# Performance work log

Measured on AMD Instinct MI355X. Metric: run time of the kernel, lower is better.

Reference implementation:

```python
import jax, jax.numpy as jnp
import numpy as np

B, S, D = 32, 4096, 64          # batch, max seq len, input_dim
P, STRIDE, H = 8, 4, 512        # patch_size, patch_stride, hidden_size
T = (S - P) // STRIDE + 1       # static max token count (sample 0 has length S)
EPS = 1e-6


def setup_inputs() -> dict:
    key = jax.random.key(0)
    k1, k2, k3 = jax.random.split(key, 3)
    x = jax.random.normal(k1, (B, S, D), dtype=jnp.float32)
    lengths = jax.random.randint(k2, (B,), P, S + 1)
    lengths = lengths.at[0].set(S)  # at least one full-length sample -> max_tokens == T
    W = jax.random.normal(k3, (P * D, H), dtype=jnp.float32) / np.sqrt(P * D)
    b = jnp.zeros((H,), dtype=jnp.float32)
    scale = jnp.ones((H,), dtype=jnp.float32)  # RMSNorm scale
    return {"x": x, "lengths": lengths, "W": W, "b": b, "scale": scale}


def _patch(x, lengths):
    # number of tokens per sample: len(range(0, max(L-P+1, 1), STRIDE))
    n_tok = jnp.where(lengths >= P, (lengths - P) // STRIDE + 1, 1)  # [B]
    # gather positions for every (token, within-patch) slot
    pos = jnp.arange(T)[:, None] * STRIDE + jnp.arange(P)[None, :]   # [T, P]
    tokens = x[:, pos, :]                                            # [B, T, P, D]
    valid = (pos[None, :, :] < lengths[:, None, None]) \
          & (jnp.arange(T)[None, :, None] < n_tok[:, None, None])    # [B, T, P]
    tokens = jnp.where(valid[..., None], tokens, 0.0)
    return tokens.reshape(B, T, P * D), n_tok


def reference(x, lengths, W, b, scale):
    tokens, token_lengths = _patch(x, lengths)        # [B, T, P*D], [B]
    h = tokens @ W + b                                # proj -> [B, T, H]
    rms = jnp.sqrt(jnp.mean(h * h, axis=-1, keepdims=True) + EPS)
    hidden = h / rms * scale                          # RMSNorm
    return hidden, token_lengths, tokens
```

## Files before the change

### kernel.cpp

```cpp
#include <hip/hip_runtime.h>
#include <hip/hip_bf16.h>

constexpr int Bc = 32, Sc = 4096, Dc = 64, Pc = 8, STRIDEc = 4, Hc = 512;
constexpr int Tc = (Sc - Pc) / STRIDEc + 1;
constexpr int Kc = Pc * Dc;
constexpr float EPSc = 1e-6f;
constexpr int PITCH = 40;

typedef __bf16 bf16x8 __attribute__((ext_vector_type(8)));
typedef unsigned short ushort8 __attribute__((ext_vector_type(8)));
typedef float f32x4 __attribute__((ext_vector_type(4)));

__device__ __forceinline__ int n_tok_of(int len) {
    return (len >= Pc) ? ((len - Pc) / STRIDEc + 1) : 1;
}

__device__ __forceinline__ unsigned short f2bf(float f) {
    unsigned u = __builtin_bit_cast(unsigned, f);
    u = (u + 0x7FFFu + ((u >> 16) & 1u)) >> 16;
    return (unsigned short)u;
}

__global__ __launch_bounds__(256) void prep_kernel(
        const float* __restrict__ W, const int* __restrict__ lengths,
        unsigned short* __restrict__ Wt, float* __restrict__ out_tl) {
    __shared__ float tile[32][33];
    const int k0 = blockIdx.x * 32, n0 = blockIdx.y * 32;
    const int r = threadIdx.x >> 3, c = (threadIdx.x & 7) * 4;
    const float4 v = *(const float4*)(W + (size_t)(k0 + r) * Hc + n0 + c);
    tile[c + 0][r] = v.x;
    tile[c + 1][r] = v.y;
    tile[c + 2][r] = v.z;
    tile[c + 3][r] = v.w;
    __syncthreads();
    ushort4 o;
    o.x = f2bf(tile[r][c + 0]);
    o.y = f2bf(tile[r][c + 1]);
    o.z = f2bf(tile[r][c + 2]);
    o.w = f2bf(tile[r][c + 3]);
    *(ushort4*)(Wt + (size_t)blockIdx.x * (Hc * 32) + (size_t)(n0 + r) * 32 + c) = o;
    if (blockIdx.x == 0 && blockIdx.y == 0 && threadIdx.x < Bc)
        out_tl[threadIdx.x] = (float)n_tok_of(lengths[threadIdx.x]);
}

__global__ __launch_bounds__(256, 2) void fused_kernel(
        const float* __restrict__ x, const int* __restrict__ lengths,
        const unsigned short* __restrict__ Wt, const float* __restrict__ bias,
        const float* __restrict__ scale, float* __restrict__ hidden,
        float* __restrict__ tokens) {
    const int b  = blockIdx.y;
    const int t0 = blockIdx.x * 64;
    const int len = lengths[b];
    const int ntok = n_tok_of(len);

    __shared__ unsigned short As[64 * PITCH];
    __shared__ unsigned short Bs[512 * PITCH];
    __shared__ float ssbuf[4][64];

    const int tid  = threadIdx.x;
    const int w    = tid >> 6;
    const int lane = tid & 63;
    const int l15  = lane & 15;
    const int quad = lane >> 4;

    f32x4 acc[4][8];
#pragma unroll
    for (int tt = 0; tt < 4; ++tt)
#pragma unroll
        for (int ct = 0; ct < 8; ++ct) acc[tt][ct] = (f32x4){0.f, 0.f, 0.f, 0.f};

    const float* xb   = x + (size_t)b * (Sc * Dc);
    float*       tokb = tokens + (size_t)b * Tc * Kc;

    int   a_r[2], a_c[2];  bool a_tv[2];  const float* a_src[2];
#pragma unroll
    for (int it = 0; it < 2; ++it) {
        const int l = tid + it * 256;
        a_r[it] = l >> 3;
        a_c[it] = (l & 7) * 4;
        const int t = t0 + a_r[it];
        a_tv[it] = (t < Tc);
        a_src[it] = xb + (size_t)t * (STRIDEc * Dc);
    }

    float4  ra[2];
    ushort8 rb[8];

#pragma unroll
    for (int it = 0; it < 2; ++it) {
        const int t = t0 + a_r[it];
        const int kk = a_c[it];
        const int pos = t * STRIDEc + (kk >> 6);
        ra[it] = make_float4(0.f, 0.f, 0.f, 0.f);
        if (a_tv[it] && t < ntok && pos < len) ra[it] = *(const float4*)(a_src[it] + kk);
    }
#pragma unroll
    for (int it = 0; it < 8; ++it)
        rb[it] = *(const ushort8*)(Wt + (size_t)(tid + it * 256) * 8);

    for (int step = 0; step < 16; ++step) {
        const int k0 = step * 32;
        if (step) __syncthreads();

#pragma unroll
        for (int it = 0; it < 2; ++it) {
            const float4 v = ra[it];
            if (a_tv[it])
                *(float4*)(tokb + (size_t)(t0 + a_r[it]) * Kc + k0 + a_c[it]) = v;
            ushort4 h4;
            h4.x = f2bf(v.x); h4.y = f2bf(v.y); h4.z = f2bf(v.z); h4.w = f2bf(v.w);
            *(ushort4*)(As + a_r[it] * PITCH + a_c[it]) = h4;
        }
#pragma unroll
        for (int it = 0; it < 8; ++it) {
            const int cc = tid + it * 256;
            *(ushort8*)(Bs + (cc >> 2) * PITCH + (cc & 3) * 8) = rb[it];
        }
        __syncthreads();

        if (step < 15) {
            const int kn = k0 + 32;
#pragma unroll
            for (int it = 0; it < 2; ++it) {
                const int t = t0 + a_r[it];
                const int kk = kn + a_c[it];
                const int pos = t * STRIDEc + (kk >> 6);
                ra[it] = make_float4(0.f, 0.f, 0.f, 0.f);
                if (a_tv[it] && t < ntok && pos < len)
                    ra[it] = *(const float4*)(a_src[it] + kk);
            }
            const unsigned short* wsrc = Wt + (size_t)(step + 1) * (Hc * 32);
#pragma unroll
            for (int it = 0; it < 8; ++it)
                rb[it] = *(const ushort8*)(wsrc + (size_t)(tid + it * 256) * 8);
        }

        bf16x8 btok[4];
#pragma unroll
        for (int tt = 0; tt < 4; ++tt)
            btok[tt] = __builtin_bit_cast(bf16x8,
                *(const ushort8*)(As + (tt * 16 + l15) * PITCH + quad * 8));
#pragma unroll
        for (int ct = 0; ct < 8; ++ct) {
            bf16x8 aW = __builtin_bit_cast(bf16x8,
                *(const ushort8*)(Bs + (w * 128 + ct * 16 + l15) * PITCH + quad * 8));
#pragma unroll
            for (int tt = 0; tt < 4; ++tt)
                acc[tt][ct] = __builtin_amdgcn_mfma_f32_16x16x32_bf16(
                    aW, btok[tt], acc[tt][ct], 0, 0, 0);
        }
    }

    float ss[4] = {0.f, 0.f, 0.f, 0.f};
#pragma unroll
    for (int ct = 0; ct < 8; ++ct) {
        const f32x4 b4 = *(const f32x4*)(bias + w * 128 + ct * 16 + quad * 4);
#pragma unroll
        for (int tt = 0; tt < 4; ++tt) {
            f32x4 h = acc[tt][ct] + b4;
            acc[tt][ct] = h;
            ss[tt] += h[0] * h[0] + h[1] * h[1] + h[2] * h[2] + h[3] * h[3];
        }
    }
#pragma unroll
    for (int tt = 0; tt < 4; ++tt) {
        float s = ss[tt];
        s += __shfl_xor(s, 16);
        s += __shfl_xor(s, 32);
        if (quad == 0) ssbuf[w][tt * 16 + l15] = s;
    }
    __syncthreads();
    float rstd[4];
#pragma unroll
    for (int tt = 0; tt < 4; ++tt) {
        const int r = tt * 16 + l15;
        const float tot = ssbuf[0][r] + ssbuf[1][r] + ssbuf[2][r] + ssbuf[3][r];
        rstd[tt] = rsqrtf(tot * (1.0f / (float)Hc) + EPSc);
    }
#pragma unroll
    for (int ct = 0; ct < 8; ++ct) {
        const f32x4 s4 = *(const f32x4*)(scale + w * 128 + ct * 16 + quad * 4);
#pragma unroll
        for (int tt = 0; tt < 4; ++tt) {
            const int t = t0 + tt * 16 + l15;
            if (t < Tc) {
                f32x4 o = acc[tt][ct] * rstd[tt] * s4;
                *(f32x4*)(hidden + ((size_t)b * Tc + t) * Hc
                          + w * 128 + ct * 16 + quad * 4) = o;
            }
        }
    }
}

extern "C" void kernel_launch(void* const* d_in, const int* in_sizes, int n_in,
                              void* d_out, int out_size, void* d_ws, size_t ws_size,
                              hipStream_t stream) {
    const float* x       = (const float*)d_in[0];
    const int*   lengths = (const int*)d_in[1];
    const float* W       = (const float*)d_in[2];
    const float* bias    = (const float*)d_in[3];
    const float* scale   = (const float*)d_in[4];

    const size_t BTH = (size_t)Bc * Tc * Hc;
    float* out    = (float*)d_out;
    float* hidden = out;
    float* tl     = out + BTH;
    float* tokens = out + BTH + Bc;

    unsigned short* Wt = (unsigned short*)d_ws;

    {
        dim3 grid(Hc / 32, Hc / 32);
        prep_kernel<<<grid, 256, 0, stream>>>(W, lengths, Wt, tl);
    }
    {
        dim3 grid(16, Bc);
        fused_kernel<<<grid, 256, 0, stream>>>(x, lengths, Wt, bias, scale,
                                               hidden, tokens);
    }
}
```

Measured before the change: 181.9 us.

## Load MFMA fragments directly from global memory, dropping LDS staging and barriers

```diff
diff --git a/kernel.cpp b/kernel.cpp
--- a/kernel.cpp
+++ b/kernel.cpp
@@ -5,11 +5,11 @@
 constexpr int Tc = (Sc - Pc) / STRIDEc + 1;
 constexpr int Kc = Pc * Dc;
 constexpr float EPSc = 1e-6f;
-constexpr int PITCH = 40;
 
 typedef __bf16 bf16x8 __attribute__((ext_vector_type(8)));
 typedef unsigned short ushort8 __attribute__((ext_vector_type(8)));
 typedef float f32x4 __attribute__((ext_vector_type(4)));
+typedef unsigned int uint4v __attribute__((ext_vector_type(4)));
 
 __device__ __forceinline__ int n_tok_of(int len) {
     return (len >= Pc) ? ((len - Pc) / STRIDEc + 1) : 1;
@@ -20,10 +20,13 @@
     u = (u + 0x7FFFu + ((u >> 16) & 1u)) >> 16;
     return (unsigned short)u;
 }
+__device__ __forceinline__ unsigned pk2bf(float lo, float hi) {
+    return (unsigned)f2bf(lo) | ((unsigned)f2bf(hi) << 16);
+}
 
 __global__ __launch_bounds__(256) void prep_kernel(
         const float* __restrict__ W, const int* __restrict__ lengths,
-        unsigned short* __restrict__ Wt, float* __restrict__ out_tl) {
+        unsigned short* __restrict__ Wfrag, float* __restrict__ out_tl) {
     __shared__ float tile[32][33];
     const int k0 = blockIdx.x * 32, n0 = blockIdx.y * 32;
     const int r = threadIdx.x >> 3, c = (threadIdx.x & 7) * 4;
@@ -38,14 +41,23 @@
     o.y = f2bf(tile[r][c + 1]);
     o.z = f2bf(tile[r][c + 2]);
     o.w = f2bf(tile[r][c + 3]);
-    *(ushort4*)(Wt + (size_t)blockIdx.x * (Hc * 32) + (size_t)(n0 + r) * 32 + c) = o;
+    const int n   = n0 + r;
+    const int kk  = k0 + c;
+    const int wv  = n >> 7;
+    const int ct  = (n >> 4) & 7;
+    const int l15 = n & 15;
+    const int stp = kk >> 5;
+    const int qd  = (kk >> 3) & 3;
+    const size_t off =
+        ((((size_t)stp * 4 + wv) * 8 + ct) * 64 + qd * 16 + l15) * 8 + (kk & 7);
+    *(ushort4*)(Wfrag + off) = o;
     if (blockIdx.x == 0 && blockIdx.y == 0 && threadIdx.x < Bc)
         out_tl[threadIdx.x] = (float)n_tok_of(lengths[threadIdx.x]);
 }
 
 __global__ __launch_bounds__(256, 2) void fused_kernel(
         const float* __restrict__ x, const int* __restrict__ lengths,
-        const unsigned short* __restrict__ Wt, const float* __restrict__ bias,
+        const unsigned short* __restrict__ Wfrag, const float* __restrict__ bias,
         const float* __restrict__ scale, float* __restrict__ hidden,
         float* __restrict__ tokens) {
     const int b  = blockIdx.y;
@@ -53,8 +65,6 @@
     const int len = lengths[b];
     const int ntok = n_tok_of(len);
 
-    __shared__ unsigned short As[64 * PITCH];
-    __shared__ unsigned short Bs[512 * PITCH];
     __shared__ float ssbuf[4][64];
 
     const int tid  = threadIdx.x;
@@ -72,82 +82,68 @@
     const float* xb   = x + (size_t)b * (Sc * Dc);
     float*       tokb = tokens + (size_t)b * Tc * Kc;
 
-    int   a_r[2], a_c[2];  bool a_tv[2];  const float* a_src[2];
+    int a_r[2], a_c[2];
 #pragma unroll
     for (int it = 0; it < 2; ++it) {
         const int l = tid + it * 256;
         a_r[it] = l >> 3;
         a_c[it] = (l & 7) * 4;
-        const int t = t0 + a_r[it];
-        a_tv[it] = (t < Tc);
-        a_src[it] = xb + (size_t)t * (STRIDEc * Dc);
-    }
-
-    float4  ra[2];
-    ushort8 rb[8];
-
-#pragma unroll
-    for (int it = 0; it < 2; ++it) {
-        const int t = t0 + a_r[it];
-        const int kk = a_c[it];
-        const int pos = t * STRIDEc + (kk >> 6);
-        ra[it] = make_float4(0.f, 0.f, 0.f, 0.f);
-        if (a_tv[it] && t < ntok && pos < len) ra[it] = *(const float4*)(a_src[it] + kk);
-    }
-#pragma unroll
-    for (int it = 0; it < 8; ++it)
-        rb[it] = *(const ushort8*)(Wt + (size_t)(tid + it * 256) * 8);
+    }
+    int ft[4];
+#pragma unroll
+    for (int tt = 0; tt < 4; ++tt) ft[tt] = t0 + tt * 16 + l15;
+
+    const unsigned short* wf = Wfrag + ((size_t)w * 8) * 512 + (size_t)lane * 8;
 
     for (int step = 0; step < 16; ++step) {
         const int k0 = step * 32;
-        if (step) __syncthreads();
 
 #pragma unroll
         for (int it = 0; it < 2; ++it) {
-            const float4 v = ra[it];
-            if (a_tv[it])
-                *(float4*)(tokb + (size_t)(t0 + a_r[it]) * Kc + k0 + a_c[it]) = v;
-            ushort4 h4;
-            h4.x = f2bf(v.x); h4.y = f2bf(v.y); h4.z = f2bf(v.z); h4.w = f2bf(v.w);
-            *(ushort4*)(As + a_r[it] * PITCH + a_c[it]) = h4;
-        }
-#pragma unroll
-        for (int it = 0; it < 8; ++it) {
-            const int cc = tid + it * 256;
-            *(ushort8*)(Bs + (cc >> 2) * PITCH + (cc & 3) * 8) = rb[it];
-        }
-        __syncthreads();
-
-        if (step < 15) {
-            const int kn = k0 + 32;
-#pragma unroll
-            for (int it = 0; it < 2; ++it) {
-                const int t = t0 + a_r[it];
-                const int kk = kn + a_c[it];
-                const int pos = t * STRIDEc + (kk >> 6);
-                ra[it] = make_float4(0.f, 0.f, 0.f, 0.f);
-                if (a_tv[it] && t < ntok && pos < len)
-                    ra[it] = *(const float4*)(a_src[it] + kk);
+            const int t = t0 + a_r[it];
+            const int kk = k0 + a_c[it];
+            const int pos = t * STRIDEc + (kk >> 6);
+            float4 v = make_float4(0.f, 0.f, 0.f, 0.f);
+            if (t < ntok && pos < len)
+                v = *(const float4*)(xb + (size_t)t * (STRIDEc * Dc) + kk);
+            if (t < Tc)
+                *(float4*)(tokb + (size_t)t * Kc + kk) = v;
+        }
+
+        ushort8 aW[8];
+        const unsigned short* wfs = wf + (size_t)step * (4 * 8 * 512);
+#pragma unroll
+        for (int ct = 0; ct < 8; ++ct)
+            aW[ct] = *(const ushort8*)(wfs + ct * 512);
+
+        bf16x8 btok[4];
+        const int kf = k0 + quad * 8;
+        const int pf = kf >> 6;
+#pragma unroll
+        for (int tt = 0; tt < 4; ++tt) {
+            const int t = ft[tt];
+            float4 f0 = make_float4(0.f, 0.f, 0.f, 0.f);
+            float4 f1 = make_float4(0.f, 0.f, 0.f, 0.f);
+            if (t < ntok && (t * STRIDEc + pf) < len) {
+                const float* src = xb + (size_t)t * (STRIDEc * Dc) + kf;
+                f0 = *(const float4*)(src);
+                f1 = *(const float4*)(src + 4);
             }
-            const unsigned short* wsrc = Wt + (size_t)(step + 1) * (Hc * 32);
-#pragma unroll
-            for (int it = 0; it < 8; ++it)
-                rb[it] = *(const ushort8*)(wsrc + (size_t)(tid + it * 256) * 8);
-        }
-
-        bf16x8 btok[4];
-#pragma unroll
-        for (int tt = 0; tt < 4; ++tt)
-            btok[tt] = __builtin_bit_cast(bf16x8,
-                *(const ushort8*)(As + (tt * 16 + l15) * PITCH + quad * 8));
+            uint4v uu;
+            uu[0] = pk2bf(f0.x, f0.y);
+            uu[1] = pk2bf(f0.z, f0.w);
+            uu[2] = pk2bf(f1.x, f1.y);
+            uu[3] = pk2bf(f1.z, f1.w);
+            btok[tt] = __builtin_bit_cast(bf16x8, uu);
+        }
+
 #pragma unroll
         for (int ct = 0; ct < 8; ++ct) {
-            bf16x8 aW = __builtin_bit_cast(bf16x8,
-                *(const ushort8*)(Bs + (w * 128 + ct * 16 + l15) * PITCH + quad * 8));
+            const bf16x8 av = __builtin_bit_cast(bf16x8, aW[ct]);
 #pragma unroll
             for (int tt = 0; tt < 4; ++tt)
                 acc[tt][ct] = __builtin_amdgcn_mfma_f32_16x16x32_bf16(
-                    aW, btok[tt], acc[tt][ct], 0, 0, 0);
+                    av, btok[tt], acc[tt][ct], 0, 0, 0);
         }
     }
 
@@ -182,7 +178,7 @@
         const f32x4 s4 = *(const f32x4*)(scale + w * 128 + ct * 16 + quad * 4);
 #pragma unroll
         for (int tt = 0; tt < 4; ++tt) {
-            const int t = t0 + tt * 16 + l15;
+            const int t = ft[tt];
             if (t < Tc) {
                 f32x4 o = acc[tt][ct] * rstd[tt] * s4;
                 *(f32x4*)(hidden + ((size_t)b * Tc + t) * Hc
@@ -207,15 +203,15 @@
     float* tl     = out + BTH;
     float* tokens = out + BTH + Bc;
 
-    unsigned short* Wt = (unsigned short*)d_ws;
+    unsigned short* Wfrag = (unsigned short*)d_ws;
 
     {
         dim3 grid(Hc / 32, Hc / 32);
-        prep_kernel<<<grid, 256, 0, stream>>>(W, lengths, Wt, tl);
+        prep_kernel<<<grid, 256, 0, stream>>>(W, lengths, Wfrag, tl);
     }
     {
         dim3 grid(16, Bc);
-        fused_kernel<<<grid, 256, 0, stream>>>(x, lengths, Wt, bias, scale,
+        fused_kernel<<<grid, 256, 0, stream>>>(x, lengths, Wfrag, bias, scale,
                                                hidden, tokens);
     }
 }
```

After: 210.9 us. 1.16x slower.
